# Kernel tuning notes

Hardware: AMD Instinct MI355X
Metric: run time of the kernel (lower is better)

## Reference

```python
import jax, jax.numpy as jnp
import numpy as np

D_MODEL = 1024
NUM_HEADS = 16
D_HEAD = D_MODEL // NUM_HEADS


def setup_inputs() -> dict:
    key = jax.random.key(0)
    ks = jax.random.split(key, 5)
    b, n = 4, 2048
    x = jax.random.normal(ks[0], (b, n, D_MODEL), dtype=jnp.float32)
    s = 1.0 / np.sqrt(D_MODEL)
    w_qkv = jax.random.normal(ks[1], (D_MODEL, 3 * D_MODEL), dtype=jnp.float32) * s
    b_qkv = jax.random.normal(ks[2], (3 * D_MODEL,), dtype=jnp.float32) * 0.01
    w_out = jax.random.normal(ks[3], (D_MODEL, D_MODEL), dtype=jnp.float32) * s
    b_out = jax.random.normal(ks[4], (D_MODEL,), dtype=jnp.float32) * 0.01
    return {"x": x, "w_qkv": w_qkv, "b_qkv": b_qkv, "w_out": w_out, "b_out": b_out}


def reference(x, w_qkv, b_qkv, w_out, b_out):
    b, n, _ = x.shape
    h, d = NUM_HEADS, D_HEAD
    scale = d ** -0.5
    qkv = x @ w_qkv + b_qkv                       # [b, n, 3*d_model]
    # split as (qkv, h, d) on the feature axis, matching 'b n (qkv h d)'
    qkv = qkv.reshape(b, n, 3, h, d).transpose(2, 0, 3, 1, 4)  # [3, b, h, n, d]
    q, k, v = qkv[0], qkv[1], qkv[2]
    dots = jnp.einsum('bhid,bhjd->bhij', q, k) * scale
    causal = jnp.tril(jnp.ones((n, n), dtype=bool))
    dots = jnp.where(causal[None, None], dots, -jnp.inf)
    attn = jax.nn.softmax(dots, axis=-1)
    out = jnp.einsum('bhij,bhjd->bhid', attn, v)
    out = out.transpose(0, 2, 1, 3).reshape(b, n, h * d)
    return out @ w_out + b_out
```

## Files before the change

### kernel.cpp

```cpp
#include <hip/hip_runtime.h>
#include <hip/hip_bf16.h>
#include <stdint.h>

typedef unsigned short u16;
typedef __attribute__((ext_vector_type(8))) short bf16x8;
typedef __attribute__((ext_vector_type(4))) float f32x4;
typedef __attribute__((ext_vector_type(16))) float f32x16;
typedef __attribute__((ext_vector_type(4))) short s16x4;
typedef __attribute__((ext_vector_type(2))) unsigned u32x2;

#define SEQ   2048
#define BATCH 4

#define MFMA16(a,b,c) __builtin_amdgcn_mfma_f32_16x16x32_bf16(a,b,c,0,0,0)
#define MFMA32(a,b,c) __builtin_amdgcn_mfma_f32_32x32x16_bf16(a,b,c,0,0,0)
#define EXP2F __builtin_amdgcn_exp2f

__device__ __forceinline__ u16 f2bf(float f) {
  union { float f; uint32_t u; } c{f};
  uint32_t r = c.u + 0x7fffu + ((c.u >> 16) & 1u);
  return (u16)(r >> 16);
}

__device__ __forceinline__ void gll16(const void* g, void* l) {
  __builtin_amdgcn_global_load_lds((const __attribute__((address_space(1))) void*)g,
                                   (__attribute__((address_space(3))) void*)l,
                                   16, 0, 0);
}

__device__ __forceinline__ void plswap(uint32_t &a, uint32_t &b) {
  u32x2 r = __builtin_amdgcn_permlane32_swap(a, b, false, false);
  a = r[0]; b = r[1];
}
__device__ __forceinline__ float xhalf_max(float v) {
  union { float f; uint32_t u; } c{v};
  u32x2 r = __builtin_amdgcn_permlane32_swap(c.u, c.u, false, false);
  union { uint32_t u; float f; } x{r[0]}, y{r[1]};
  return fmaxf(x.f, y.f);
}
__device__ __forceinline__ float xhalf_add(float v) {
  union { float f; uint32_t u; } c{v};
  u32x2 r = __builtin_amdgcn_permlane32_swap(c.u, c.u, false, false);
  union { uint32_t u; float f; } x{r[0]}, y{r[1]};
  return x.f + y.f;
}

__global__ __launch_bounds__(256) void k_prep(const float* __restrict__ x,
                                              u16* __restrict__ xbf,
                                              const float* __restrict__ wqkv,
                                              u16* __restrict__ wqkvT,
                                              const float* __restrict__ wout,
                                              u16* __restrict__ woutT) {
  __shared__ float tl[32][33];
  const int bid = blockIdx.x, t = threadIdx.x;
  if (bid < 4096) {
    int i = (bid * 256 + t) * 8;
    float4 a = *(const float4*)(x + i);
    float4 b = *(const float4*)(x + i + 4);
    union { u16 u[8]; bf16x8 v; } r;
    r.u[0] = f2bf(a.x); r.u[1] = f2bf(a.y); r.u[2] = f2bf(a.z); r.u[3] = f2bf(a.w);
    r.u[4] = f2bf(b.x); r.u[5] = f2bf(b.y); r.u[6] = f2bf(b.z); r.u[7] = f2bf(b.w);
    *(bf16x8*)(xbf + i) = r.v;
    return;
  }
  const float* in; u16* out; int N, idx, nx;
  if (bid < 4096 + 3072) { in = wqkv; out = wqkvT; N = 3072; idx = bid - 4096; nx = 96; }
  else                   { in = wout; out = woutT; N = 1024; idx = bid - 7168; nx = 32; }
  const int K = 1024;
  const int c0 = (idx % nx) * 32, r0 = (idx / nx) * 32;
  const int tx = t & 31, ty = t >> 5;
#pragma unroll
  for (int j = 0; j < 32; j += 8)
    tl[ty + j][tx] = in[(size_t)(r0 + ty + j) * N + c0 + tx];
  __syncthreads();
#pragma unroll
  for (int j = 0; j < 32; j += 8)
    out[(size_t)(c0 + ty + j) * K + r0 + tx] = f2bf(tl[tx][ty + j]);
}

#define SBAR  asm volatile("s_barrier" ::: "memory")
#define LGKM0 asm volatile("s_waitcnt lgkmcnt(0)" ::: "memory")
#define VM2   asm volatile("s_waitcnt vmcnt(2)" ::: "memory")
#define VM0   asm volatile("s_waitcnt vmcnt(0)" ::: "memory")
#define FEN   asm volatile("" ::: "memory")

template<int OUT_F32, int VSPLIT>
__global__ __launch_bounds__(512, 2) void k_gemm256(const u16* __restrict__ A,
                                                    const u16* __restrict__ BT,
                                                    const float* __restrict__ bias,
                                                    void* __restrict__ Cv,
                                                    u16* __restrict__ vT,
                                                    int N, int K, int NT, int TN) {
  __shared__ alignas(16) char LDS[98304];
  const int t = threadIdx.x;
  const int l = t & 63, w = t >> 6;
  const int wm = w >> 2, wn = w & 3;
  const int lr = l & 15, lg = l >> 4;

  const int nwg = gridDim.x;
  const int cpx = nwg >> 3;
  const int sb = (blockIdx.x & 7) * cpx + (blockIdx.x >> 3);
  const int brow = (sb / TN) * 256, bcol = (sb % TN) * 128;

  auto stageA = [&](int c, int h, int tt) {
#pragma unroll
    for (int i = 0; i < 2; i++) {
      int s = t + i * 512;
      int r = s >> 3, cg = s & 7;
      int grow = brow + (r >> 6) * 128 + h * 64 + (r & 63);
      int gk = tt * 64 + ((cg ^ (r & 7)) * 8);
      gll16(A + (size_t)grow * K + gk, LDS + c * 49152 + h * 16384 + s * 16);
    }
  };
  auto stageB = [&](int c, int tt) {
#pragma unroll
    for (int i = 0; i < 2; i++) {
      int s = t + i * 512;
      int r = s >> 3, cg = s & 7;
      int grow = bcol + r;
      int gk = tt * 64 + ((cg ^ (r & 7)) * 8);
      gll16(BT + (size_t)grow * K + gk, LDS + c * 49152 + 32768 + s * 16);
    }
  };

  f32x4 acc[8][2] = {};
  bf16x8 afr[4], bfr[2];

#define READ_A(c, h, ks)                                                       \
  {                                                                            \
    const char* baseA = LDS + (c) * 49152 + (h) * 16384 + (wm * 64) * 128;     \
    _Pragma("unroll") for (int mi = 0; mi < 4; mi++)                           \
      afr[mi] = *(const bf16x8*)(baseA + (mi * 16 + lr) * 128 +                \
                                 ((((ks) * 4 + lg) ^ (lr & 7)) * 16));         \
  }
#define READ_B(c, ks)                                                          \
  {                                                                            \
    const char* baseB = LDS + (c) * 49152 + 32768 + (wn * 32) * 128;           \
    _Pragma("unroll") for (int ni = 0; ni < 2; ni++)                           \
      bfr[ni] = *(const bf16x8*)(baseB + (ni * 16 + lr) * 128 +                \
                                 ((((ks) * 4 + lg) ^ (lr & 7)) * 16));         \
  }
#define DO_MFMA(H)                                                             \
  {                                                                            \
    __builtin_amdgcn_s_setprio(1);                                             \
    _Pragma("unroll") for (int mi = 0; mi < 4; mi++)                           \
      _Pragma("unroll") for (int ni = 0; ni < 2; ni++)                         \
        acc[(H)*4 + mi][ni] = MFMA16(afr[mi], bfr[ni], acc[(H)*4 + mi][ni]);   \
    __builtin_amdgcn_s_setprio(0);                                             \
  }

  stageA(0, 0, 0); FEN;
  stageB(0, 0);    FEN;
  stageA(0, 1, 0); FEN;
  VM2; SBAR;

  for (int tt = 0; tt < NT; tt++) {
    const int c = tt & 1;
    if (tt + 1 < NT) { stageA(c ^ 1, 0, tt + 1); FEN; }
    READ_A(c, 0, 0); READ_B(c, 0);
    DO_MFMA(0);
    if (tt + 1 < NT) { VM2; } else { VM0; }
    LGKM0; SBAR;
    if (tt + 1 < NT) { stageB(c ^ 1, tt + 1); FEN; }
    READ_A(c, 1, 0);
    DO_MFMA(1);
    if (tt + 1 < NT) { stageA(c ^ 1, 1, tt + 1); FEN; }
    READ_A(c, 1, 1); READ_B(c, 1);
    DO_MFMA(1);
    READ_A(c, 0, 1);
    DO_MFMA(0);
    VM2;
    LGKM0; SBAR;
  }

  const int r0 = brow + wm * 128 + lg * 4;
  const int c0 = bcol + wn * 32 + lr;
#pragma unroll
  for (int ni = 0; ni < 2; ni++) {
    const int col = c0 + ni * 16;
    float bv = bias[col];
#pragma unroll
    for (int mig = 0; mig < 8; mig++) {
      const int row = r0 + mig * 16;
      if (VSPLIT && col >= 2048) {
        const int bb = row >> 11, n0 = row & 2047;
        union { u16 u[4]; s16x4 v; } pk4;
#pragma unroll
        for (int r = 0; r < 4; r++) pk4.u[r] = f2bf(acc[mig][ni][r] + bv);
        *(s16x4*)(vT + ((size_t)(bb * 1024 + col - 2048) * SEQ + n0)) = pk4.v;
      } else {
#pragma unroll
        for (int r = 0; r < 4; r++) {
          float v = acc[mig][ni][r] + bv;
          size_t off = (size_t)(row + r) * N + col;
          if (OUT_F32) ((float*)Cv)[off] = v;
          else         ((u16*)Cv)[off]   = f2bf(v);
        }
      }
    }
  }
}
#undef READ_A
#undef READ_B
#undef DO_MFMA

__global__ __launch_bounds__(256) void k_attn(const u16* __restrict__ qkv,
                                              const u16* __restrict__ vT,
                                              u16* __restrict__ outp) {
  __shared__ alignas(16) char SB[2][16384];
  const int t = threadIdx.x, l = t & 63, w = t >> 6;
  const int hi = l >> 5, q = l & 31;
  const int h = blockIdx.x, qp = blockIdx.y, b = blockIdx.z;
  const int bh = b * 16 + h;
  const int srow = t >> 3;
  const int csw = ((t & 7) * 16) ^ ((srow & 7) << 4);
  const int swz = (q & 7) << 4;
  const float SC = 0.18033688011112042f;

  auto STAGE = [&](char* buf, int kv0) {
    char* lK = buf + w * 1024;
    char* lV = buf + 8192 + w * 1024;
    gll16(qkv + (size_t)(b * SEQ + kv0 + srow) * 3072 + 1024 + h * 64 + (csw >> 1), lK);
    gll16(qkv + (size_t)(b * SEQ + kv0 + srow + 32) * 3072 + 1024 + h * 64 + (csw >> 1), lK + 4096);
    gll16(vT + (size_t)(bh * 64 + srow) * SEQ + kv0 + (csw >> 1), lV);
    gll16(vT + (size_t)(bh * 64 + srow + 32) * SEQ + kv0 + (csw >> 1), lV + 4096);
  };

  for (int tsel = 0; tsel < 2; tsel++) {
    const int qt = tsel ? (15 - qp) : qp;
    const int qr0 = qt * 128 + w * 32;
    const int qg = qr0 + q;
    bf16x8 qf[4];
#pragma unroll
    for (int c = 0; c < 4; c++)
      qf[c] = *(const bf16x8*)(qkv + (size_t)(b * SEQ + qg) * 3072 + h * 64 + c * 16 + hi * 8);
    f32x16 o0 = {}, o1 = {}, lv = {};
    float m_run = -1e30f;
    const int nkv = 2 * qt + 2;

    STAGE(SB[0], 0);
    for (int j = 0; j < nkv; j++) {
      const int kv0 = j * 64;
      __syncthreads();
      if (j + 1 < nkv) STAGE(SB[(j + 1) & 1], kv0 + 64);
      const char* Kb = SB[j & 1];
      const char* Vb = Kb + 8192;

      if (kv0 <= qr0 + 31) {
        f32x16 st0 = {}, st1 = {};
        __builtin_amdgcn_s_setprio(1);
#pragma unroll
        for (int c = 0; c < 4; c++) {
          const int cb = c * 32 + hi * 16;
          bf16x8 k0 = *(const bf16x8*)(Kb + q * 128 + (cb ^ swz));
          bf16x8 k1 = *(const bf16x8*)(Kb + (32 + q) * 128 + (cb ^ swz));
          st0 = MFMA32(k0, qf[c], st0);
          st1 = MFMA32(k1, qf[c], st1);
        }
        __builtin_amdgcn_s_setprio(0);
        if (kv0 + 63 > qr0) {
#pragma unroll
          for (int r = 0; r < 16; r++) {
            const int krow = (r & 3) + 8 * (r >> 2) + 4 * hi;
            if (kv0 + krow > qg)      st0[r] = -1e30f;
            if (kv0 + 32 + krow > qg) st1[r] = -1e30f;
          }
        }
        float tmx[16];
#pragma unroll
        for (int r = 0; r < 16; r++) tmx[r] = fmaxf(st0[r], st1[r]);
        float v0 = fmaxf(fmaxf(tmx[0], tmx[1]), tmx[2]);
        float v1 = fmaxf(fmaxf(tmx[3], tmx[4]), tmx[5]);
        float v2 = fmaxf(fmaxf(tmx[6], tmx[7]), tmx[8]);
        float v3 = fmaxf(fmaxf(tmx[9], tmx[10]), tmx[11]);
        float v4 = fmaxf(fmaxf(tmx[12], tmx[13]), tmx[14]);
        float v5 = fmaxf(fmaxf(v0, v1), tmx[15]);
        float v6 = fmaxf(fmaxf(v2, v3), v4);
        float v7 = fmaxf(v5, v6);
        const float vs = xhalf_max(v7) * SC;
        if (__any(vs > m_run + 8.0f)) {
          float mnew = fmaxf(m_run, vs);
          float corr = EXP2F(m_run - mnew);
          m_run = mnew;
#pragma unroll
          for (int r = 0; r < 16; r++) { o0[r] *= corr; o1[r] *= corr; lv[r] *= corr; }
        }
        f32x16 e0 = st0 * SC - m_run;
        f32x16 e1 = st1 * SC - m_run;
        f32x16 p0, p1;
#pragma unroll
        for (int r = 0; r < 16; r++) { p0[r] = EXP2F(e0[r]); p1[r] = EXP2F(e1[r]); }
        lv += p0 + p1;
#pragma unroll
        for (int khb = 0; khb < 2; khb++) {
          uint32_t pk[8];
#pragma unroll
          for (int ii = 0; ii < 8; ii++) {
            float lo = khb ? p1[2 * ii] : p0[2 * ii];
            float hf = khb ? p1[2 * ii + 1] : p0[2 * ii + 1];
            asm("v_cvt_pk_bf16_f32 %0, %1, %2" : "=v"(pk[ii]) : "v"(lo), "v"(hf));
          }
          plswap(pk[0], pk[2]); plswap(pk[1], pk[3]);
          plswap(pk[4], pk[6]); plswap(pk[5], pk[7]);
          union { uint32_t u[4]; bf16x8 v; } be, bo;
          be.u[0] = pk[0]; be.u[1] = pk[1]; be.u[2] = pk[2]; be.u[3] = pk[3];
          bo.u[0] = pk[4]; bo.u[1] = pk[5]; bo.u[2] = pk[6]; bo.u[3] = pk[7];
          __builtin_amdgcn_s_setprio(1);
#pragma unroll
          for (int kti = 0; kti < 2; kti++) {
            const int cb = (khb * 2 + kti) * 32 + hi * 16;
            bf16x8 vv0 = *(const bf16x8*)(Vb + q * 128 + (cb ^ swz));
            bf16x8 vv1 = *(const bf16x8*)(Vb + (32 + q) * 128 + (cb ^ swz));
            bf16x8 pb = kti ? bo.v : be.v;
            o0 = MFMA32(vv0, pb, o0);
            o1 = MFMA32(vv1, pb, o1);
          }
          __builtin_amdgcn_s_setprio(0);
        }
      }
    }
    __syncthreads();
    float ls = ((lv[0] + lv[1]) + (lv[2] + lv[3])) + ((lv[4] + lv[5]) + (lv[6] + lv[7]))
             + ((lv[8] + lv[9]) + (lv[10] + lv[11])) + ((lv[12] + lv[13]) + (lv[14] + lv[15]));
    ls = xhalf_add(ls);
    const float invl = 1.0f / ls;
#pragma unroll
    for (int dh = 0; dh < 2; dh++)
#pragma unroll
      for (int jq = 0; jq < 4; jq++) {
        union { u16 u[4]; s16x4 v; } pk4;
#pragma unroll
        for (int r = 0; r < 4; r++)
          pk4.u[r] = f2bf((dh ? o1[4 * jq + r] : o0[4 * jq + r]) * invl);
        *(s16x4*)(outp + (size_t)(b * SEQ + qg) * 1024 + h * 64 + dh * 32 + jq * 8 + hi * 4) = pk4.v;
      }
  }
}

extern "C" void kernel_launch(void* const* d_in, const int* in_sizes, int n_in,
                              void* d_out, int out_size, void* d_ws, size_t ws_size,
                              hipStream_t stream) {
  const float* x     = (const float*)d_in[0];
  const float* w_qkv = (const float*)d_in[1];
  const float* b_qkv = (const float*)d_in[2];
  const float* w_out = (const float*)d_in[3];
  const float* b_out = (const float*)d_in[4];

  char* ws = (char*)d_ws;
  u16* xbf   = (u16*)(ws);
  u16* wqkvT = (u16*)(ws + (16u << 20));
  u16* woutT = (u16*)(ws + (22u << 20));
  u16* qkvb  = (u16*)(ws + (24u << 20));
  u16* vTb   = (u16*)(ws + (72u << 20));

  k_prep<<<8192, 256, 0, stream>>>(x, xbf, w_qkv, wqkvT, w_out, woutT);
  k_gemm256<0, 1><<<768, 512, 0, stream>>>(xbf, wqkvT, b_qkv, qkvb, vTb, 3072, 1024, 16, 24);
  k_attn<<<dim3(16, 8, 4), 256, 0, stream>>>(qkvb, vTb, xbf);
  k_gemm256<1, 0><<<256, 512, 0, stream>>>(xbf, woutT, b_out, d_out, nullptr, 1024, 1024, 16, 8);
}
```

Baseline: 168.9 us.

## Process both paired query tiles in one KV sweep to share K/V staging

```diff
diff --git a/kernel.cpp b/kernel.cpp
--- a/kernel.cpp
+++ b/kernel.cpp
@@ -204,9 +204,9 @@
 #undef READ_B
 #undef DO_MFMA
 
-__global__ __launch_bounds__(256) void k_attn(const u16* __restrict__ qkv,
-                                              const u16* __restrict__ vT,
-                                              u16* __restrict__ outp) {
+__global__ __launch_bounds__(256, 2) void k_attn(const u16* __restrict__ qkv,
+                                                 const u16* __restrict__ vT,
+                                                 u16* __restrict__ outp) {
   __shared__ alignas(16) char SB[2][16384];
   const int t = threadIdx.x, l = t & 63, w = t >> 6;
   const int hi = l >> 5, q = l & 31;
@@ -226,100 +226,113 @@
     gll16(vT + (size_t)(bh * 64 + srow + 32) * SEQ + kv0 + (csw >> 1), lV + 4096);
   };
 
-  for (int tsel = 0; tsel < 2; tsel++) {
-    const int qt = tsel ? (15 - qp) : qp;
-    const int qr0 = qt * 128 + w * 32;
-    const int qg = qr0 + q;
-    bf16x8 qf[4];
-#pragma unroll
-    for (int c = 0; c < 4; c++)
-      qf[c] = *(const bf16x8*)(qkv + (size_t)(b * SEQ + qg) * 3072 + h * 64 + c * 16 + hi * 8);
-    f32x16 o0 = {}, o1 = {}, lv = {};
-    float m_run = -1e30f;
-    const int nkv = 2 * qt + 2;
-
-    STAGE(SB[0], 0);
-    for (int j = 0; j < nkv; j++) {
-      const int kv0 = j * 64;
-      __syncthreads();
-      if (j + 1 < nkv) STAGE(SB[(j + 1) & 1], kv0 + 64);
-      const char* Kb = SB[j & 1];
-      const char* Vb = Kb + 8192;
-
-      if (kv0 <= qr0 + 31) {
-        f32x16 st0 = {}, st1 = {};
-        __builtin_amdgcn_s_setprio(1);
-#pragma unroll
-        for (int c = 0; c < 4; c++) {
-          const int cb = c * 32 + hi * 16;
-          bf16x8 k0 = *(const bf16x8*)(Kb + q * 128 + (cb ^ swz));
-          bf16x8 k1 = *(const bf16x8*)(Kb + (32 + q) * 128 + (cb ^ swz));
-          st0 = MFMA32(k0, qf[c], st0);
-          st1 = MFMA32(k1, qf[c], st1);
-        }
-        __builtin_amdgcn_s_setprio(0);
-        if (kv0 + 63 > qr0) {
-#pragma unroll
-          for (int r = 0; r < 16; r++) {
-            const int krow = (r & 3) + 8 * (r >> 2) + 4 * hi;
-            if (kv0 + krow > qg)      st0[r] = -1e30f;
-            if (kv0 + 32 + krow > qg) st1[r] = -1e30f;
-          }
-        }
-        float tmx[16];
-#pragma unroll
-        for (int r = 0; r < 16; r++) tmx[r] = fmaxf(st0[r], st1[r]);
-        float v0 = fmaxf(fmaxf(tmx[0], tmx[1]), tmx[2]);
-        float v1 = fmaxf(fmaxf(tmx[3], tmx[4]), tmx[5]);
-        float v2 = fmaxf(fmaxf(tmx[6], tmx[7]), tmx[8]);
-        float v3 = fmaxf(fmaxf(tmx[9], tmx[10]), tmx[11]);
-        float v4 = fmaxf(fmaxf(tmx[12], tmx[13]), tmx[14]);
-        float v5 = fmaxf(fmaxf(v0, v1), tmx[15]);
-        float v6 = fmaxf(fmaxf(v2, v3), v4);
-        float v7 = fmaxf(v5, v6);
-        const float vs = xhalf_max(v7) * SC;
-        if (__any(vs > m_run + 8.0f)) {
-          float mnew = fmaxf(m_run, vs);
-          float corr = EXP2F(m_run - mnew);
-          m_run = mnew;
-#pragma unroll
-          for (int r = 0; r < 16; r++) { o0[r] *= corr; o1[r] *= corr; lv[r] *= corr; }
-        }
-        f32x16 e0 = st0 * SC - m_run;
-        f32x16 e1 = st1 * SC - m_run;
-        f32x16 p0, p1;
-#pragma unroll
-        for (int r = 0; r < 16; r++) { p0[r] = EXP2F(e0[r]); p1[r] = EXP2F(e1[r]); }
-        lv += p0 + p1;
-#pragma unroll
-        for (int khb = 0; khb < 2; khb++) {
-          uint32_t pk[8];
-#pragma unroll
-          for (int ii = 0; ii < 8; ii++) {
-            float lo = khb ? p1[2 * ii] : p0[2 * ii];
-            float hf = khb ? p1[2 * ii + 1] : p0[2 * ii + 1];
-            asm("v_cvt_pk_bf16_f32 %0, %1, %2" : "=v"(pk[ii]) : "v"(lo), "v"(hf));
-          }
-          plswap(pk[0], pk[2]); plswap(pk[1], pk[3]);
-          plswap(pk[4], pk[6]); plswap(pk[5], pk[7]);
-          union { uint32_t u[4]; bf16x8 v; } be, bo;
-          be.u[0] = pk[0]; be.u[1] = pk[1]; be.u[2] = pk[2]; be.u[3] = pk[3];
-          bo.u[0] = pk[4]; bo.u[1] = pk[5]; bo.u[2] = pk[6]; bo.u[3] = pk[7];
-          __builtin_amdgcn_s_setprio(1);
-#pragma unroll
-          for (int kti = 0; kti < 2; kti++) {
-            const int cb = (khb * 2 + kti) * 32 + hi * 16;
-            bf16x8 vv0 = *(const bf16x8*)(Vb + q * 128 + (cb ^ swz));
-            bf16x8 vv1 = *(const bf16x8*)(Vb + (32 + q) * 128 + (cb ^ swz));
-            bf16x8 pb = kti ? bo.v : be.v;
-            o0 = MFMA32(vv0, pb, o0);
-            o1 = MFMA32(vv1, pb, o1);
-          }
-          __builtin_amdgcn_s_setprio(0);
-        }
-      }
-    }
+  auto COMPUTE = [&](const char* Kb, const char* Vb, int kv0, int qr0, int qg,
+                     const bf16x8* qf, f32x16& o0, f32x16& o1, f32x16& lv,
+                     float& m_run) {
+    f32x16 st0 = {}, st1 = {};
+    __builtin_amdgcn_s_setprio(1);
+#pragma unroll
+    for (int c = 0; c < 4; c++) {
+      const int cb = c * 32 + hi * 16;
+      bf16x8 k0 = *(const bf16x8*)(Kb + q * 128 + (cb ^ swz));
+      bf16x8 k1 = *(const bf16x8*)(Kb + (32 + q) * 128 + (cb ^ swz));
+      st0 = MFMA32(k0, qf[c], st0);
+      st1 = MFMA32(k1, qf[c], st1);
+    }
+    __builtin_amdgcn_s_setprio(0);
+    if (kv0 + 63 > qr0) {
+#pragma unroll
+      for (int r = 0; r < 16; r++) {
+        const int krow = (r & 3) + 8 * (r >> 2) + 4 * hi;
+        if (kv0 + krow > qg)      st0[r] = -1e30f;
+        if (kv0 + 32 + krow > qg) st1[r] = -1e30f;
+      }
+    }
+    float tmx[16];
+#pragma unroll
+    for (int r = 0; r < 16; r++) tmx[r] = fmaxf(st0[r], st1[r]);
+    float v0 = fmaxf(fmaxf(tmx[0], tmx[1]), tmx[2]);
+    float v1 = fmaxf(fmaxf(tmx[3], tmx[4]), tmx[5]);
+    float v2 = fmaxf(fmaxf(tmx[6], tmx[7]), tmx[8]);
+    float v3 = fmaxf(fmaxf(tmx[9], tmx[10]), tmx[11]);
+    float v4 = fmaxf(fmaxf(tmx[12], tmx[13]), tmx[14]);
+    float v5 = fmaxf(fmaxf(v0, v1), tmx[15]);
+    float v6 = fmaxf(fmaxf(v2, v3), v4);
+    float v7 = fmaxf(v5, v6);
+    const float vs = xhalf_max(v7) * SC;
+    if (__any(vs > m_run + 8.0f)) {
+      float mnew = fmaxf(m_run, vs);
+      float corr = EXP2F(m_run - mnew);
+      m_run = mnew;
+#pragma unroll
+      for (int r = 0; r < 16; r++) { o0[r] *= corr; o1[r] *= corr; lv[r] *= corr; }
+    }
+    f32x16 e0 = st0 * SC - m_run;
+    f32x16 e1 = st1 * SC - m_run;
+    f32x16 p0, p1;
+#pragma unroll
+    for (int r = 0; r < 16; r++) { p0[r] = EXP2F(e0[r]); p1[r] = EXP2F(e1[r]); }
+    lv += p0 + p1;
+#pragma unroll
+    for (int khb = 0; khb < 2; khb++) {
+      uint32_t pk[8];
+#pragma unroll
+      for (int ii = 0; ii < 8; ii++) {
+        float lo = khb ? p1[2 * ii] : p0[2 * ii];
+        float hf = khb ? p1[2 * ii + 1] : p0[2 * ii + 1];
+        asm("v_cvt_pk_bf16_f32 %0, %1, %2" : "=v"(pk[ii]) : "v"(lo), "v"(hf));
+      }
+      plswap(pk[0], pk[2]); plswap(pk[1], pk[3]);
+      plswap(pk[4], pk[6]); plswap(pk[5], pk[7]);
+      union { uint32_t u[4]; bf16x8 v; } be, bo;
+      be.u[0] = pk[0]; be.u[1] = pk[1]; be.u[2] = pk[2]; be.u[3] = pk[3];
+      bo.u[0] = pk[4]; bo.u[1] = pk[5]; bo.u[2] = pk[6]; bo.u[3] = pk[7];
+      __builtin_amdgcn_s_setprio(1);
+#pragma unroll
+      for (int kti = 0; kti < 2; kti++) {
+        const int cb = (khb * 2 + kti) * 32 + hi * 16;
+        bf16x8 vv0 = *(const bf16x8*)(Vb + q * 128 + (cb ^ swz));
+        bf16x8 vv1 = *(const bf16x8*)(Vb + (32 + q) * 128 + (cb ^ swz));
+        bf16x8 pb = kti ? bo.v : be.v;
+        o0 = MFMA32(vv0, pb, o0);
+        o1 = MFMA32(vv1, pb, o1);
+      }
+      __builtin_amdgcn_s_setprio(0);
+    }
+  };
+
+  const int qtA = qp, qtB = 15 - qp;
+  const int qr0A = qtA * 128 + w * 32, qgA = qr0A + q;
+  const int qr0B = qtB * 128 + w * 32, qgB = qr0B + q;
+  bf16x8 qfA[4], qfB[4];
+#pragma unroll
+  for (int c = 0; c < 4; c++) {
+    qfA[c] = *(const bf16x8*)(qkv + (size_t)(b * SEQ + qgA) * 3072 + h * 64 + c * 16 + hi * 8);
+    qfB[c] = *(const bf16x8*)(qkv + (size_t)(b * SEQ + qgB) * 3072 + h * 64 + c * 16 + hi * 8);
+  }
+  f32x16 oA0 = {}, oA1 = {}, lvA = {};
+  f32x16 oB0 = {}, oB1 = {}, lvB = {};
+  float mA = -1e30f, mB = -1e30f;
+  const int nkvB = 2 * qtB + 2;
+
+  STAGE(SB[0], 0);
+  for (int j = 0; j < nkvB; j++) {
+    const int kv0 = j * 64;
     __syncthreads();
+    if (j + 1 < nkvB) STAGE(SB[(j + 1) & 1], kv0 + 64);
+    const char* Kb = SB[j & 1];
+    const char* Vb = Kb + 8192;
+    if (kv0 <= qr0A + 31)
+      COMPUTE(Kb, Vb, kv0, qr0A, qgA, qfA, oA0, oA1, lvA, mA);
+    if (kv0 <= qr0B + 31)
+      COMPUTE(Kb, Vb, kv0, qr0B, qgB, qfB, oB0, oB1, lvB, mB);
+  }
+#pragma unroll
+  for (int sel = 0; sel < 2; sel++) {
+    f32x16& o0 = sel ? oB0 : oA0;
+    f32x16& o1 = sel ? oB1 : oA1;
+    f32x16& lv = sel ? lvB : lvA;
+    const int qg = sel ? qgB : qgA;
     float ls = ((lv[0] + lv[1]) + (lv[2] + lv[3])) + ((lv[4] + lv[5]) + (lv[6] + lv[7]))
              + ((lv[8] + lv[9]) + (lv[10] + lv[11])) + ((lv[12] + lv[13]) + (lv[14] + lv[15]));
     ls = xhalf_add(ls);
```

New measurement: 160.0 us. 5.3% less time.
